# Kernel tuning notes

Hardware: AMD Instinct MI355X
Metric: run time of the kernel (lower is better)

The kernel has to match this reference:

```python
import jax, jax.numpy as jnp
import numpy as np


def setup_inputs() -> dict:
    key = jax.random.key(0)
    N, E, H, V, C, D, L = 10000, 50000, 128, 8, 5, 59, 2
    keys = iter(jax.random.split(key, 64))

    def p(*shape):
        return jax.random.normal(next(keys), shape, jnp.float32) * 0.05

    inp = dict(
        edge_index=jax.random.randint(next(keys), (2, E), 0, N),
        edge_attr=jax.random.normal(next(keys), (E, D), jnp.float32),
        delta_t=jnp.array([60.0], jnp.float32),
        memory=jnp.ones((N, H), jnp.float32),
        # edge_embed
        W_ee=p(H, D), b_ee=p(H),
        # edge_weight_gen
        W_ewg=p(V, 2 * H), b_ewg=p(V),
        # multi-view GIN convs (L layers, shared MLP across views)
        gin_W1=p(L, H, H), gin_b1=p(L, H), gin_W2=p(L, H, H), gin_b2=p(L, H),
        # Bochner time encoder
        W_t=p(H, 1), b_t=p(H),
        # GRUCell (torch gate order r,z,n)
        W_ih=p(3 * H, H), b_ih=p(3 * H), W_hh=p(3 * H, H), b_hh=p(3 * H),
        # update_nn (feeds detached memory only; not in returned outputs)
        W_up=p(H, V * H), b_up=p(H),
        # local attention (kdim=vdim=2H, 1 head)
        Wq_l=p(H, H), bq_l=p(H), Wk_l=p(H, 2 * H), bk_l=p(H),
        Wv_l=p(H, 2 * H), bv_l=p(H), Wo_l=p(H, H), bo_l=p(H),
        # global attention (1 head)
        Wq_g=p(H, H), bq_g=p(H), Wk_g=p(H, H), bk_g=p(H),
        Wv_g=p(H, H), bv_g=p(H), Wo_g=p(H, H), bo_g=p(H),
        # classifier MLP
        Wc1=p(H, 3 * H), bc1=p(H), Wc2=p(C, H), bc2=p(C),
    )
    return inp


def reference(edge_index, edge_attr, delta_t, memory,
              W_ee, b_ee, W_ewg, b_ewg,
              gin_W1, gin_b1, gin_W2, gin_b2,
              W_t, b_t, W_ih, b_ih, W_hh, b_hh, W_up, b_up,
              Wq_l, bq_l, Wk_l, bk_l, Wv_l, bv_l, Wo_l, bo_l,
              Wq_g, bq_g, Wk_g, bk_g, Wv_g, bv_g, Wo_g, bo_g,
              Wc1, bc1, Wc2, bc2):
    relu = jax.nn.relu
    N, H = memory.shape
    V = W_ewg.shape[0]
    L = gin_W1.shape[0]

    # ---- snapshot encoder (MultiGraphLayer) ----
    ea = relu(edge_attr @ W_ee.T + b_ee)                               # [E,H]
    src0, dst0 = edge_index[0], edge_index[1]
    ew = jax.nn.sigmoid(
        jnp.concatenate([ea, memory[src0]], -1) @ W_ewg.T + b_ewg)     # [E,V]
    h = jnp.broadcast_to(memory[:, None, :], (N, V, H))                # [N,V,H]
    cs, cd = dst0, src0  # edge_index flipped before convs (edge_index[[1,0]])
    for l in range(L):
        # multi-view GIN: view-weighted message + residual MLP update
        msg = relu(h[cs] + ea[:, None, :]) * ew[:, :, None]            # [E,V,H]
        agg = jax.ops.segment_sum(msg, cd, num_segments=N)             # [N,V,H]
        upd = relu((h + agg) @ gin_W1[l].T + gin_b1[l]) @ gin_W2[l].T + gin_b2[l]
        h = h + upd
    h_before = h

    # ---- GRU memory update (vectorized over the V 'class' slots) ----
    te = jnp.sin(delta_t[:, None] * W_t[:, 0] + b_t)                   # [1,H]
    x_in = h + te                                                      # [N,V,H]
    gi = x_in @ W_ih.T + b_ih                                          # [N,V,3H]
    gh = (memory @ W_hh.T + b_hh)[:, None, :]                          # [N,1,3H]
    r = jax.nn.sigmoid(gi[..., :H] + gh[..., :H])
    z = jax.nn.sigmoid(gi[..., H:2 * H] + gh[..., H:2 * H])
    n = jnp.tanh(gi[..., 2 * H:] + r * gh[..., 2 * H:])
    h_new = (1.0 - z) * n + z * memory[:, None, :]                     # [N,V,H]

    # ---- global/local attention fusion ----
    scale = 1.0 / jnp.sqrt(jnp.asarray(H, jnp.float32))
    sf, df = h_new[src0], h_new[dst0]                                  # [E,V,H]
    Wk1, Wk2 = Wk_l[:, :H], Wk_l[:, H:]  # split cat([src,dst]) projection
    Wv1, Wv2 = Wv_l[:, :H], Wv_l[:, H:]
    q_l = ea @ Wq_l.T + bq_l                                           # [E,H]
    K_l = sf @ Wk1.T + df @ Wk2.T + bk_l                               # [E,V,H]
    V_l = sf @ Wv1.T + df @ Wv2.T + bv_l
    a_l = jax.nn.softmax(jnp.einsum('eh,evh->ev', q_l, K_l) * scale, -1)
    local_out = jnp.einsum('ev,evh->eh', a_l, V_l) @ Wo_l.T + bo_l     # [E,H]

    pooled = h_new.mean(axis=0)                                        # [V,H]
    q_g = ea @ Wq_g.T + bq_g
    K_g = pooled @ Wk_g.T + bk_g
    V_g = pooled @ Wv_g.T + bv_g
    a_g = jax.nn.softmax((q_g @ K_g.T) * scale, axis=-1)               # [E,V]
    global_out = (a_g @ V_g) @ Wo_g.T + bo_g                           # [E,H]

    combined = jnp.concatenate([ea, local_out, global_out], axis=-1)   # [E,3H]
    logits = relu(combined @ Wc1.T + bc1) @ Wc2.T + bc2                # [E,C]
    return (logits, ew, h_before, a_g[:, None, :])
```

## Files before the change

### kernel.cpp

```cpp
#include <hip/hip_runtime.h>
#include <cstddef>


#define HSZ 128
typedef unsigned short ushortT;
typedef unsigned int uintT;
typedef short short8 __attribute__((ext_vector_type(8)));
typedef float f32x4 __attribute__((ext_vector_type(4)));

__device__ __forceinline__ float sigm(float x) { return 1.f / (1.f + __expf(-x)); }

__device__ __forceinline__ ushortT f2bf(float f) {
  unsigned int u = __float_as_uint(f);
  u += 0x7fffu + ((u >> 16) & 1u);
  return (ushortT)(u >> 16);
}
__device__ __forceinline__ float bf2f(ushortT u) {
  return __uint_as_float(((unsigned int)u) << 16);
}
__device__ __forceinline__ float bflo(uintT u) { return __uint_as_float(u << 16); }
__device__ __forceinline__ float bfhi(uintT u) { return __uint_as_float(u & 0xffff0000u); }
__device__ __forceinline__ uintT pk2bf(float a, float b) {
  return ((uintT)f2bf(b) << 16) | (uintT)f2bf(a);
}

__device__ __forceinline__ int swzA(int row, int chunk) {
  return row * 64 + (((chunk ^ row) & 7) << 3);
}
__device__ __forceinline__ int swzT(int row, int chunk) {
  return row * 128 + (((chunk & 8) | ((chunk ^ row) & 7)) << 3);
}

template<int ASRC, int ACT, bool OUTBF, bool ABF, bool WBF>
__global__ __launch_bounds__(256) void gemm_bf(
    const void* __restrict__ A1, const void* __restrict__ A2, const void* __restrict__ A3,
    const void* __restrict__ W, const float* __restrict__ bias,
    void* __restrict__ out_, int M, int K, int Nout)
{
  __shared__ short Ash[128 * 64];
  __shared__ short Bsh[128 * 64];
  float* out = (float*)out_;
  ushortT* outh = (ushortT*)out_;
  const int tid = threadIdx.x;
  const int m0 = blockIdx.x * 128;
  const int n0 = blockIdx.y * 128;
  const int l = tid & 63, w = tid >> 6;
  const int wr = w >> 1, wc = w & 1;
  const int lr = l & 15, lq = l >> 4;
  f32x4 acc[4][4] = {};

  for (int k0 = 0; k0 < K; k0 += 64) {
    __syncthreads();
    const bool fast = (k0 + 64 <= K);
    #pragma unroll
    for (int i = 0; i < 4; ++i) {
      int c = i * 256 + tid;
      int row = c >> 3, seg = c & 7;
      int kb = k0 + seg * 8;
      {
        int m = m0 + row;
        short8 pk;
        if (ABF) {
          if (m < M) {
            if (ASRC == 3) {
              const ushortT* S = (kb < 128) ? (const ushortT*)A1
                               : (kb < 256) ? (const ushortT*)A2 : (const ushortT*)A3;
              pk = *reinterpret_cast<const short8*>(S + (size_t)m * 128 + (kb & 127));
            } else {
              pk = *reinterpret_cast<const short8*>((const ushortT*)A1 + (size_t)m * K + kb);
            }
          } else {
            #pragma unroll
            for (int j = 0; j < 8; ++j) pk[j] = 0;
          }
        } else {
          const float* A1f = (const float*)A1;
          float v[8];
          if (fast && m < M) {
            const float4* p = reinterpret_cast<const float4*>(A1f + (size_t)m * K + kb);
            float4 x0 = p[0], x1 = p[1];
            v[0]=x0.x; v[1]=x0.y; v[2]=x0.z; v[3]=x0.w;
            v[4]=x1.x; v[5]=x1.y; v[6]=x1.z; v[7]=x1.w;
          } else {
            #pragma unroll
            for (int j = 0; j < 8; ++j) {
              int k = kb + j;
              v[j] = (m < M && k < K) ? A1f[(size_t)m * K + k] : 0.f;
            }
          }
          #pragma unroll
          for (int j = 0; j < 8; ++j) pk[j] = (short)f2bf(v[j]);
        }
        *reinterpret_cast<short8*>(&Ash[swzA(row, seg)]) = pk;
      }
      {
        int nn = n0 + row;
        short8 pk;
        if (WBF) {
          if (nn < Nout)
            pk = *reinterpret_cast<const short8*>((const ushortT*)W + (size_t)nn * K + kb);
          else {
            #pragma unroll
            for (int j = 0; j < 8; ++j) pk[j] = 0;
          }
        } else {
          const float* Wf = (const float*)W;
          float v[8];
          if (fast && nn < Nout) {
            const float4* p = reinterpret_cast<const float4*>(Wf + (size_t)nn * K + kb);
            float4 x0 = p[0], x1 = p[1];
            v[0]=x0.x; v[1]=x0.y; v[2]=x0.z; v[3]=x0.w;
            v[4]=x1.x; v[5]=x1.y; v[6]=x1.z; v[7]=x1.w;
          } else {
            #pragma unroll
            for (int j = 0; j < 8; ++j) {
              int k = kb + j;
              v[j] = (nn < Nout && k < K) ? Wf[(size_t)nn * K + k] : 0.f;
            }
          }
          #pragma unroll
          for (int j = 0; j < 8; ++j) pk[j] = (short)f2bf(v[j]);
        }
        *reinterpret_cast<short8*>(&Bsh[swzA(row, seg)]) = pk;
      }
    }
    __syncthreads();
    #pragma unroll
    for (int ks = 0; ks < 2; ++ks) {
      short8 a[4], b[4];
      #pragma unroll
      for (int mi = 0; mi < 4; ++mi)
        a[mi] = *reinterpret_cast<const short8*>(&Ash[swzA(wr*64 + mi*16 + lr, ks*4 + lq)]);
      #pragma unroll
      for (int ni = 0; ni < 4; ++ni)
        b[ni] = *reinterpret_cast<const short8*>(&Bsh[swzA(wc*64 + ni*16 + lr, ks*4 + lq)]);
      #pragma unroll
      for (int mi = 0; mi < 4; ++mi)
        #pragma unroll
        for (int ni = 0; ni < 4; ++ni)
          acc[mi][ni] = __builtin_amdgcn_mfma_f32_16x16x32_bf16(a[mi], b[ni], acc[mi][ni], 0, 0, 0);
    }
  }
  #pragma unroll
  for (int ni = 0; ni < 4; ++ni) {
    int col = n0 + wc*64 + ni*16 + lr;
    if (col >= Nout) continue;
    float bz = bias ? bias[col] : 0.f;
    #pragma unroll
    for (int mi = 0; mi < 4; ++mi) {
      int mb = m0 + wr*64 + mi*16 + lq*4;
      #pragma unroll
      for (int r = 0; r < 4; ++r) {
        int m = mb + r;
        if (m >= M) continue;
        float vv = acc[mi][ni][r] + bz;
        if (ACT == 1) vv = fmaxf(vv, 0.f);
        size_t o = (size_t)m * Nout + col;
        if (OUTBF) outh[o] = f2bf(vv); else out[o] = vv;
      }
    }
  }
}

template<int LMODE>
__global__ __launch_bounds__(256) void k_gin(
    const ushortT* __restrict__ hb, const ushortT* __restrict__ aggb,
    float* __restrict__ houtf, ushortT* __restrict__ houtb,
    const ushortT* __restrict__ W1b, const float* __restrict__ b1,
    const ushortT* __restrict__ W2b, const float* __restrict__ b2, int M)
{
  __shared__ short smem[24576];
  short* Ash  = smem;
  short* Bsh  = smem + 8192;
  short* Tsh  = smem;
  short* B2sh = smem + 16384;
  const int tid = threadIdx.x;
  const int m0 = blockIdx.x * 128;
  const int l = tid & 63, w = tid >> 6;
  const int wr = w >> 1, wc = w & 1;
  const int lr = l & 15, lq = l >> 4;
  f32x4 acc[4][4] = {};

  for (int ks2 = 0; ks2 < 2; ++ks2) {
    if (ks2) __syncthreads();
    #pragma unroll
    for (int i = 0; i < 4; ++i) {
      int c = i * 256 + tid;
      int row = c >> 3, seg = c & 7;
      int kb = ks2 * 64 + seg * 8;
      {
        int m = m0 + row;
        short8 pk;
        if (m < M) {
          short8 hv;
          if (LMODE == 1) hv = *reinterpret_cast<const short8*>(hb + ((size_t)(m >> 3)) * 128 + kb);
          else            hv = *reinterpret_cast<const short8*>(hb + (size_t)m * 128 + kb);
          short8 av = *reinterpret_cast<const short8*>(aggb + (size_t)m * 128 + kb);
          #pragma unroll
          for (int j = 0; j < 8; ++j)
            pk[j] = (short)f2bf(bf2f((ushortT)hv[j]) + bf2f((ushortT)av[j]));
        } else {
          #pragma unroll
          for (int j = 0; j < 8; ++j) pk[j] = 0;
        }
        *reinterpret_cast<short8*>(&Ash[swzA(row, seg)]) = pk;
      }
      *reinterpret_cast<short8*>(&Bsh[swzA(row, seg)]) =
          *reinterpret_cast<const short8*>(W1b + (size_t)row * 128 + kb);
      if (ks2 == 0)
        *reinterpret_cast<short8*>(&B2sh[swzA(row, seg)]) =
            *reinterpret_cast<const short8*>(W2b + (size_t)row * 128 + seg * 8);
    }
    __syncthreads();
    #pragma unroll
    for (int ks = 0; ks < 2; ++ks) {
      short8 a[4], b[4];
      #pragma unroll
      for (int mi = 0; mi < 4; ++mi)
        a[mi] = *reinterpret_cast<const short8*>(&Ash[swzA(wr*64 + mi*16 + lr, ks*4 + lq)]);
      #pragma unroll
      for (int ni = 0; ni < 4; ++ni)
        b[ni] = *reinterpret_cast<const short8*>(&Bsh[swzA(wc*64 + ni*16 + lr, ks*4 + lq)]);
      #pragma unroll
      for (int mi = 0; mi < 4; ++mi)
        #pragma unroll
        for (int ni = 0; ni < 4; ++ni)
          acc[mi][ni] = __builtin_amdgcn_mfma_f32_16x16x32_bf16(a[mi], b[ni], acc[mi][ni], 0, 0, 0);
    }
  }
  __syncthreads();
  {
    float b1v[4];
    #pragma unroll
    for (int ni = 0; ni < 4; ++ni) b1v[ni] = b1[wc*64 + ni*16 + lr];
    #pragma unroll
    for (int mi = 0; mi < 4; ++mi)
      #pragma unroll
      for (int ni = 0; ni < 4; ++ni) {
        int col = wc*64 + ni*16 + lr;
        #pragma unroll
        for (int r = 0; r < 4; ++r) {
          int row = wr*64 + mi*16 + lq*4 + r;
          float v = fmaxf(acc[mi][ni][r] + b1v[ni], 0.f);
          Tsh[swzT(row, col >> 3) + (col & 7)] = (short)f2bf(v);
        }
      }
  }
  __syncthreads();
  f32x4 acc2[4][4] = {};
  for (int ks2 = 0; ks2 < 2; ++ks2) {
    if (ks2) {
      __syncthreads();
      #pragma unroll
      for (int i = 0; i < 4; ++i) {
        int c = i * 256 + tid;
        int row = c >> 3, seg = c & 7;
        *reinterpret_cast<short8*>(&B2sh[swzA(row, seg)]) =
            *reinterpret_cast<const short8*>(W2b + (size_t)row * 128 + 64 + seg * 8);
      }
      __syncthreads();
    }
    #pragma unroll
    for (int ks = 0; ks < 2; ++ks) {
      short8 a[4], b[4];
      #pragma unroll
      for (int mi = 0; mi < 4; ++mi)
        a[mi] = *reinterpret_cast<const short8*>(&Tsh[swzT(wr*64 + mi*16 + lr, ks2*8 + ks*4 + lq)]);
      #pragma unroll
      for (int ni = 0; ni < 4; ++ni)
        b[ni] = *reinterpret_cast<const short8*>(&B2sh[swzA(wc*64 + ni*16 + lr, ks*4 + lq)]);
      #pragma unroll
      for (int mi = 0; mi < 4; ++mi)
        #pragma unroll
        for (int ni = 0; ni < 4; ++ni)
          acc2[mi][ni] = __builtin_amdgcn_mfma_f32_16x16x32_bf16(a[mi], b[ni], acc2[mi][ni], 0, 0, 0);
    }
  }
  {
    float b2v[4];
    #pragma unroll
    for (int ni = 0; ni < 4; ++ni) b2v[ni] = b2[wc*64 + ni*16 + lr];
    #pragma unroll
    for (int ni = 0; ni < 4; ++ni) {
      int col = wc*64 + ni*16 + lr;
      #pragma unroll
      for (int mi = 0; mi < 4; ++mi) {
        int mb = m0 + wr*64 + mi*16 + lq*4;
        #pragma unroll
        for (int r = 0; r < 4; ++r) {
          int m = mb + r;
          if (m >= M) continue;
          float base = (LMODE == 1) ? bf2f(hb[((size_t)(m >> 3)) * 128 + col])
                                    : bf2f(hb[(size_t)m * 128 + col]);
          float ho = base + acc2[mi][ni][r] + b2v[ni];
          if (LMODE == 1) houtb[(size_t)m * 128 + col] = f2bf(ho);
          else            houtf[(size_t)m * 128 + col] = ho;
        }
      }
    }
  }
}

__global__ __launch_bounds__(512) void k_giru(
    const float* __restrict__ hf, const float* __restrict__ te,
    const ushortT* __restrict__ Wihb, const float* __restrict__ b_ih,
    const ushortT* __restrict__ ghb, const ushortT* __restrict__ memb,
    ushortT* __restrict__ hnb, int M)
{
  __shared__ short Ash[8192];
  __shared__ short Bsh[24576];
  const int tid = threadIdx.x;
  const int m0 = blockIdx.x * 64;
  const int l = tid & 63, w = tid >> 6;
  const int lr = l & 15, lq = l >> 4;
  const int r0 = (w >> 1) * 16, c0 = (w & 1) * 64;
  f32x4 acc[3][4] = {};

  #pragma unroll
  for (int i = 0; i < 2; ++i) {
    int c = i * 512 + tid;
    int row = c >> 4, seg = c & 15;
    int m = m0 + row;
    short8 pk;
    if (m < M) {
      const float4* p = reinterpret_cast<const float4*>(hf + (size_t)m * 128 + seg * 8);
      const float4* t = reinterpret_cast<const float4*>(te + seg * 8);
      float4 x0 = p[0], x1 = p[1], t0 = t[0], t1 = t[1];
      pk[0]=(short)f2bf(x0.x+t0.x); pk[1]=(short)f2bf(x0.y+t0.y);
      pk[2]=(short)f2bf(x0.z+t0.z); pk[3]=(short)f2bf(x0.w+t0.w);
      pk[4]=(short)f2bf(x1.x+t1.x); pk[5]=(short)f2bf(x1.y+t1.y);
      pk[6]=(short)f2bf(x1.z+t1.z); pk[7]=(short)f2bf(x1.w+t1.w);
    } else {
      #pragma unroll
      for (int j = 0; j < 8; ++j) pk[j] = 0;
    }
    *reinterpret_cast<short8*>(&Ash[swzT(row, seg)]) = pk;
  }
  for (int ks2 = 0; ks2 < 2; ++ks2) {
    if (ks2) __syncthreads();
    #pragma unroll
    for (int i = 0; i < 6; ++i) {
      int c = i * 512 + tid;
      int row = c >> 3, seg = c & 7;
      *reinterpret_cast<short8*>(&Bsh[swzA(row, seg)]) =
          *reinterpret_cast<const short8*>(Wihb + (size_t)row * 128 + ks2 * 64 + seg * 8);
    }
    __syncthreads();
    #pragma unroll
    for (int ks = 0; ks < 2; ++ks) {
      short8 a = *reinterpret_cast<const short8*>(&Ash[swzT(r0 + lr, ks2*8 + ks*4 + lq)]);
      #pragma unroll
      for (int s = 0; s < 3; ++s)
        #pragma unroll
        for (int xi = 0; xi < 4; ++xi) {
          short8 b = *reinterpret_cast<const short8*>(
              &Bsh[swzA(s*128 + c0 + xi*16 + lr, ks*4 + lq)]);
          acc[s][xi] = __builtin_amdgcn_mfma_f32_16x16x32_bf16(a, b, acc[s][xi], 0, 0, 0);
        }
    }
  }
  #pragma unroll
  for (int xi = 0; xi < 4; ++xi) {
    int x = c0 + xi * 16 + lr;
    float br = b_ih[x], bz = b_ih[128 + x], bn = b_ih[256 + x];
    #pragma unroll
    for (int rr = 0; rr < 4; ++rr) {
      int m = m0 + r0 + lq * 4 + rr;
      if (m >= M) continue;
      int node = m >> 3;
      float ghr = bf2f(ghb[(size_t)node * 384 + x]);
      float ghz = bf2f(ghb[(size_t)node * 384 + 128 + x]);
      float ghn = bf2f(ghb[(size_t)node * 384 + 256 + x]);
      float mem = bf2f(memb[(size_t)node * 128 + x]);
      float rv = sigm(acc[0][xi][rr] + br + ghr);
      float zv = sigm(acc[1][xi][rr] + bz + ghz);
      float nv = tanhf(acc[2][xi][rr] + bn + rv * ghn);
      hnb[(size_t)m * 128 + x] = f2bf((1.f - zv) * nv + zv * mem);
    }
  }
}

__global__ void k_hist(const int* __restrict__ srcI, int* __restrict__ cnt, int E)
{
  int e = blockIdx.x * 256 + threadIdx.x;
  if (e < E) atomicAdd(&cnt[srcI[e]], 1);
}

__global__ __launch_bounds__(1024) void k_scan(const int* __restrict__ cnt,
    int* __restrict__ ofs, int* __restrict__ cur, int N)
{
  __shared__ int buf[1024];
  __shared__ int carry;
  int tid = threadIdx.x;
  if (tid == 0) carry = 0;
  __syncthreads();
  for (int base = 0; base < N; base += 1024) {
    int i = base + tid;
    int v = (i < N) ? cnt[i] : 0;
    buf[tid] = v;
    __syncthreads();
    for (int off = 1; off < 1024; off <<= 1) {
      int t = (tid >= off) ? buf[tid - off] : 0;
      __syncthreads();
      buf[tid] += t;
      __syncthreads();
    }
    int excl = carry + buf[tid] - v;
    if (i < N) { ofs[i] = excl; cur[i] = excl; }
    __syncthreads();
    if (tid == 0) carry += buf[1023];
    __syncthreads();
  }
  if (tid == 0) ofs[N] = carry;
}

__global__ void k_fill(const int* __restrict__ srcI, int* __restrict__ cur,
                       int* __restrict__ eid, int E)
{
  int e = blockIdx.x * 256 + threadIdx.x;
  if (e >= E) return;
  int p = atomicAdd(&cur[srcI[e]], 1);
  eid[p] = e;
}

template<int LMODE>
__global__ __launch_bounds__(256) void k_agg(const ushortT* __restrict__ hb,
    const ushortT* __restrict__ eab, const float* __restrict__ ew,
    const int* __restrict__ dstI, const int* __restrict__ ofs,
    const int* __restrict__ eid, ushortT* __restrict__ aggb, int N)
{
  int half = threadIdx.x >> 7;
  int x = threadIdx.x & 127;
  int n = blockIdx.x * 2 + half;
  if (n >= N) return;
  float acc[8] = {};
  int beg = ofs[n], end = ofs[n + 1];
  for (int i = beg; i < end; ++i) {
    int e = eid[i];
    int d = dstI[e];
    float eav = bf2f(eab[(size_t)e * 128 + x]);
    const float* ewp = ew + (size_t)e * 8;
    if (LMODE == 1) {
      float m = fmaxf(bf2f(hb[(size_t)d * 128 + x]) + eav, 0.f);
      #pragma unroll
      for (int v = 0; v < 8; ++v) acc[v] += m * ewp[v];
    } else {
      const ushortT* hd = hb + (size_t)d * 1024;
      #pragma unroll
      for (int v = 0; v < 8; ++v)
        acc[v] += fmaxf(bf2f(hd[v * 128 + x]) + eav, 0.f) * ewp[v];
    }
  }
  ushortT* ag = aggb + (size_t)n * 1024;
  #pragma unroll
  for (int v = 0; v < 8; ++v) ag[v * 128 + x] = f2bf(acc[v]);
}

__global__ __launch_bounds__(256) void k_ew(const ushortT* __restrict__ eab,
    const ushortT* __restrict__ memb, const int* __restrict__ srcI,
    const float* __restrict__ W_ewg, const float* __restrict__ b_ewg,
    float* __restrict__ ew, int E)
{
  __shared__ float Wsh[2048];
  __shared__ float bsh[8];
  int tid = threadIdx.x;
  for (int i = tid; i < 2048; i += 256) Wsh[i] = W_ewg[i];
  if (tid < 8) bsh[tid] = b_ewg[tid];
  __syncthreads();
  int wv = tid >> 6, lane = tid & 63;
  int e = blockIdx.x * 4 + wv;
  if (e >= E) return;
  int s = srcI[e];
  float c0 = bf2f(eab[(size_t)e * 128 + lane]);
  float c1 = bf2f(eab[(size_t)e * 128 + 64 + lane]);
  float c2 = bf2f(memb[(size_t)s * 128 + lane]);
  float c3 = bf2f(memb[(size_t)s * 128 + 64 + lane]);
  #pragma unroll
  for (int v = 0; v < 8; ++v) {
    float p = c0 * Wsh[v * 256 + lane] + c1 * Wsh[v * 256 + 64 + lane]
            + c2 * Wsh[v * 256 + 128 + lane] + c3 * Wsh[v * 256 + 192 + lane];
    #pragma unroll
    for (int o = 32; o; o >>= 1) p += __shfl_down(p, o);
    if (lane == 0) ew[(size_t)e * 8 + v] = sigm(p + bsh[v]);
  }
}

__global__ void k_cvt(const float* __restrict__ src, ushortT* __restrict__ dst, int total)
{
  int i = blockIdx.x * 256 + threadIdx.x;
  if (i < total) dst[i] = f2bf(src[i]);
}

__global__ void k_te(const float* __restrict__ delta_t, const float* __restrict__ W_t,
                     const float* __restrict__ b_t, float* __restrict__ te)
{
  int t = threadIdx.x;
  if (t < 128) te[t] = sinf(delta_t[0] * W_t[t] + b_t[t]);
}

__global__ __launch_bounds__(256) void k_pool(const ushortT* __restrict__ hnb,
                                              float* __restrict__ prw, int N)
{
  int tid = threadIdx.x;
  float acc[4] = {0.f, 0.f, 0.f, 0.f};
  for (int n = blockIdx.x; n < N; n += gridDim.x) {
    const ushortT* row = hnb + (size_t)n * 1024;
    #pragma unroll
    for (int j = 0; j < 4; ++j) acc[j] += bf2f(row[tid + j * 256]);
  }
  #pragma unroll
  for (int j = 0; j < 4; ++j) atomicAdd(&prw[tid + j * 256], acc[j]);
}

__global__ __launch_bounds__(256) void k_prep(
    const float* __restrict__ Wo_l, const float* __restrict__ Wv_l,
    const float* __restrict__ bv_l, const float* __restrict__ bo_l,
    const float* __restrict__ Wq_l, const float* __restrict__ bq_l,
    const float* __restrict__ Wk_l, const float* __restrict__ Wq_g,
    const float* __restrict__ bq_g,
    ushortT* __restrict__ Wl2b, float* __restrict__ blv,
    ushortT* __restrict__ Wqkgb, float* __restrict__ bqkg)
{
  int idx = blockIdx.x * 256 + threadIdx.x;
  if (idx < 32768) {
    int n = idx >> 8, k = idx & 255;
    float a = 0.f;
    for (int j = 0; j < 128; ++j) a += Wo_l[n * 128 + j] * Wv_l[j * 256 + k];
    Wl2b[idx] = f2bf(a);
  } else if (idx < 65536) {
    int rem = idx - 32768;
    int n = rem >> 7, j = rem & 127;
    float a = 0.f;
    for (int k = 0; k < 128; ++k) a += Wq_l[k * 128 + j] * Wk_l[k * 256 + n];
    Wqkgb[rem] = f2bf(a);
  } else {
    int rem = idx - 65536;
    Wqkgb[32768 + rem] = f2bf(Wq_g[rem]);
  }
  if (blockIdx.x == 0 && threadIdx.x < 128) {
    int n = threadIdx.x;
    float a = bo_l[n];
    for (int j = 0; j < 128; ++j) a += Wo_l[n * 128 + j] * bv_l[j];
    blv[n] = a;
  }
  if (blockIdx.x == 1) {
    int n = threadIdx.x;
    float a = 0.f;
    for (int k = 0; k < 128; ++k) a += bq_l[k] * Wk_l[k * 256 + n];
    bqkg[n] = a;
  }
  if (blockIdx.x == 2 && threadIdx.x < 128) bqkg[256 + threadIdx.x] = bq_g[threadIdx.x];
}

__global__ __launch_bounds__(256) void k_kgg(const float* __restrict__ prw,
    const float* __restrict__ Wk_g, const float* __restrict__ Wv_g, const float* __restrict__ bv_g,
    const float* __restrict__ Wo_g, float* __restrict__ Kg, float* __restrict__ G, int N)
{
  __shared__ float pl[1024];
  __shared__ float vg[1024];
  int tid = threadIdx.x;
  float invN = 1.f / (float)N;
  for (int i = tid; i < 1024; i += 256) pl[i] = prw[i] * invN;
  __syncthreads();
  for (int o = tid; o < 1024; o += 256) {
    int v = o >> 7, x = o & 127;
    float a = 0.f, b = 0.f;
    for (int k = 0; k < 128; ++k) {
      float p = pl[v * 128 + k];
      a += p * Wk_g[(size_t)x * 128 + k];
      b += p * Wv_g[(size_t)x * 128 + k];
    }
    Kg[o] = a;
    vg[o] = b + bv_g[x];
  }
  __syncthreads();
  for (int o = tid; o < 1024; o += 256) {
    int v = o >> 7, x = o & 127;
    float a = 0.f;
    for (int k = 0; k < 128; ++k) a += vg[v * 128 + k] * Wo_g[(size_t)x * 128 + k];
    G[o] = a;
  }
}

__global__ __launch_bounds__(256) void k_lg(
    const ushortT* __restrict__ hnb, const ushortT* __restrict__ qkgb,
    const int* __restrict__ srcI, const int* __restrict__ dstI,
    const float* __restrict__ Kg, const float* __restrict__ G,
    const float* __restrict__ bo_g,
    float* __restrict__ ag_out, ushortT* __restrict__ wsd,
    ushortT* __restrict__ glbb, int E)
{
  __shared__ float Kgs[1024], Gs[1024], bs[128];
  int tid = threadIdx.x;
  for (int i = tid; i < 1024; i += 256) { Kgs[i] = Kg[i]; Gs[i] = G[i]; }
  if (tid < 128) bs[tid] = bo_g[tid];
  __syncthreads();
  int w = tid >> 6, l = tid & 63;
  int e = blockIdx.x * 4 + w;
  if (e >= E) return;
  int s = srcI[e], d = dstI[e];
  const uintT* qrow = reinterpret_cast<const uintT*>(qkgb + (size_t)e * 384);
  const uintT* srow = reinterpret_cast<const uintT*>(hnb + (size_t)s * 1024);
  const uintT* drow = reinterpret_cast<const uintT*>(hnb + (size_t)d * 1024);
  uintT q1u = qrow[l], q2u = qrow[64 + l], qgu = qrow[128 + l];
  float q1a = bflo(q1u), q1b = bfhi(q1u);
  float q2a = bflo(q2u), q2b = bfhi(q2u);
  float qga = bflo(qgu), qgb_ = bfhi(qgu);
  float sfa[8], sfb[8], dfa[8], dfb[8], pl[8], pg[8];
  #pragma unroll
  for (int v = 0; v < 8; ++v) {
    uintT su = srow[v * 64 + l], du = drow[v * 64 + l];
    sfa[v] = bflo(su); sfb[v] = bfhi(su);
    dfa[v] = bflo(du); dfb[v] = bfhi(du);
    pl[v] = q1a * sfa[v] + q1b * sfb[v] + q2a * dfa[v] + q2b * dfb[v];
    float2 kv = *reinterpret_cast<const float2*>(&Kgs[v * 128 + 2 * l]);
    pg[v] = qga * kv.x + qgb_ * kv.y;
  }
  #pragma unroll
  for (int v = 0; v < 8; ++v) {
    #pragma unroll
    for (int m = 1; m <= 32; m <<= 1) {
      pl[v] += __shfl_xor(pl[v], m);
      pg[v] += __shfl_xor(pg[v], m);
    }
  }
  const float scale = 0.08838834764831845f;
  float mx = pl[0];
  #pragma unroll
  for (int v = 1; v < 8; ++v) mx = fmaxf(mx, pl[v]);
  float suml = 0.f, al[8];
  #pragma unroll
  for (int v = 0; v < 8; ++v) { al[v] = __expf((pl[v] - mx) * scale); suml += al[v]; }
  float invl = 1.f / suml;
  float wsa = 0.f, wsb = 0.f, wda = 0.f, wdb = 0.f;
  #pragma unroll
  for (int v = 0; v < 8; ++v) {
    float a = al[v];
    wsa += a * sfa[v]; wsb += a * sfb[v];
    wda += a * dfa[v]; wdb += a * dfb[v];
  }
  uintT* wrow = reinterpret_cast<uintT*>(wsd + (size_t)e * 256);
  wrow[l]      = pk2bf(wsa * invl, wsb * invl);
  wrow[64 + l] = pk2bf(wda * invl, wdb * invl);
  float mg = pg[0];
  #pragma unroll
  for (int v = 1; v < 8; ++v) mg = fmaxf(mg, pg[v]);
  float sumg = 0.f, ag[8];
  #pragma unroll
  for (int v = 0; v < 8; ++v) { ag[v] = __expf((pg[v] - mg) * scale); sumg += ag[v]; }
  float invg = 1.f / sumg;
  if (l < 8) ag_out[(size_t)e * 8 + l] = ag[l] * invg;
  float2 bv = *reinterpret_cast<const float2*>(&bs[2 * l]);
  float ga = bv.x, gb = bv.y;
  #pragma unroll
  for (int v = 0; v < 8; ++v) {
    float sv = ag[v] * invg;
    float2 gv = *reinterpret_cast<const float2*>(&Gs[v * 128 + 2 * l]);
    ga += sv * gv.x; gb += sv * gv.y;
  }
  reinterpret_cast<uintT*>(glbb)[(size_t)e * 64 + l] = pk2bf(ga, gb);
}

__global__ __launch_bounds__(256) void k_logits(const ushortT* __restrict__ hid,
    const float* __restrict__ Wc2, const float* __restrict__ bc2,
    float* __restrict__ logits, int E)
{
  __shared__ float Wsh[640];
  __shared__ float bsh[5];
  int tid = threadIdx.x;
  for (int i = tid; i < 640; i += 256) Wsh[i] = Wc2[i];
  if (tid < 5) bsh[tid] = bc2[tid];
  __syncthreads();
  int wv = tid >> 6, lane = tid & 63;
  int e = blockIdx.x * 4 + wv;
  if (e >= E) return;
  float h0 = bf2f(hid[(size_t)e * 128 + lane]), h1 = bf2f(hid[(size_t)e * 128 + 64 + lane]);
  #pragma unroll
  for (int c = 0; c < 5; ++c) {
    float p = h0 * Wsh[c * 128 + lane] + h1 * Wsh[c * 128 + 64 + lane];
    #pragma unroll
    for (int o = 32; o; o >>= 1) p += __shfl_down(p, o);
    if (lane == 0) logits[(size_t)e * 5 + c] = p + bsh[c];
  }
}

extern "C" void kernel_launch(void* const* d_in, const int* in_sizes, int n_in,
                              void* d_out, int out_size, void* d_ws, size_t ws_size,
                              hipStream_t stream)
{
  const int*   edge_index = (const int*)d_in[0];
  const float* edge_attr  = (const float*)d_in[1];
  const float* delta_t    = (const float*)d_in[2];
  const float* memory     = (const float*)d_in[3];
  const float* W_ee  = (const float*)d_in[4];
  const float* b_ee  = (const float*)d_in[5];
  const float* W_ewg = (const float*)d_in[6];
  const float* b_ewg = (const float*)d_in[7];
  const float* gin_W1 = (const float*)d_in[8];
  const float* gin_b1 = (const float*)d_in[9];
  const float* gin_W2 = (const float*)d_in[10];
  const float* gin_b2 = (const float*)d_in[11];
  const float* W_t  = (const float*)d_in[12];
  const float* b_t  = (const float*)d_in[13];
  const float* W_ih = (const float*)d_in[14];
  const float* b_ih = (const float*)d_in[15];
  const float* W_hh = (const float*)d_in[16];
  const float* b_hh = (const float*)d_in[17];
  const float* Wq_l = (const float*)d_in[20];
  const float* bq_l = (const float*)d_in[21];
  const float* Wk_l = (const float*)d_in[22];
  const float* Wv_l = (const float*)d_in[24];
  const float* bv_l = (const float*)d_in[25];
  const float* Wo_l = (const float*)d_in[26];
  const float* bo_l = (const float*)d_in[27];
  const float* Wq_g = (const float*)d_in[28];
  const float* bq_g = (const float*)d_in[29];
  const float* Wk_g = (const float*)d_in[30];
  const float* Wv_g = (const float*)d_in[32];
  const float* bv_g = (const float*)d_in[33];
  const float* Wo_g = (const float*)d_in[34];
  const float* bo_g = (const float*)d_in[35];
  const float* Wc1  = (const float*)d_in[36];
  const float* bc1  = (const float*)d_in[37];
  const float* Wc2  = (const float*)d_in[38];
  const float* bc2  = (const float*)d_in[39];

  const int E = in_sizes[0] / 2;
  const int N = in_sizes[3] / HSZ;
  const int* srcI = edge_index;
  const int* dstI = edge_index + E;

  float* out    = (float*)d_out;
  float* logits = out;
  float* ew     = out + (size_t)E * 5;
  float* h      = out + (size_t)E * 13;
  float* ag_out = out + (size_t)E * 13 + (size_t)N * 1024;

  float* ws = (float*)d_ws;
  size_t off = 0;
  auto alloc = [&](size_t n) { size_t o = off; off += (n + 255) & ~(size_t)255; return o; };
  float* te   = ws + alloc(128);
  float* blv  = ws + alloc(128);
  float* bqkg = ws + alloc(384);
  float* Kg   = ws + alloc(1024);
  float* G    = ws + alloc(1024);
  float* prw  = ws + alloc(1024);
  int* cnt = (int*)(ws + alloc(N));
  int* ofs = (int*)(ws + alloc(N + 1));
  int* cur = (int*)(ws + alloc(N));
  int* eid = (int*)(ws + alloc(E));
  ushortT* memb   = (ushortT*)(ws + alloc((size_t)N * 64));
  ushortT* eab    = (ushortT*)(ws + alloc((size_t)E * 64));
  ushortT* h1b    = (ushortT*)(ws + alloc((size_t)N * 512));
  ushortT* hnb    = (ushortT*)(ws + alloc((size_t)N * 512));
  ushortT* ghb    = (ushortT*)(ws + alloc((size_t)N * 192));
  ushortT* ginW1b = (ushortT*)(ws + alloc(16384));
  ushortT* ginW2b = (ushortT*)(ws + alloc(16384));
  ushortT* Wihb   = (ushortT*)(ws + alloc(24576));
  ushortT* Wc1b   = (ushortT*)(ws + alloc(24576));
  ushortT* Wl2b   = (ushortT*)(ws + alloc(16384));
  ushortT* Wqkgb  = (ushortT*)(ws + alloc(24576));
  size_t brA = (size_t)N * 512, brC = (size_t)E * 448;
  size_t brsz = brA > brC ? brA : brC;
  float* BR = ws + alloc(brsz);
  if (ws_size < off * sizeof(float)) return;

  ushortT* aggb = (ushortT*)BR;
  ushortT* qkgb = (ushortT*)BR;
  ushortT* wsd  = (ushortT*)(BR + (size_t)E * 192);
  ushortT* lclb = (ushortT*)(BR + (size_t)E * 320);
  ushortT* glbb = (ushortT*)(BR + (size_t)E * 384);
  ushortT* hid  = (ushortT*)BR;

  auto cdiv = [](int a, int b) { return (a + b - 1) / b; };

  hipMemsetAsync(cnt, 0, (size_t)N * sizeof(int), stream);
  k_hist<<<cdiv(E, 256), 256, 0, stream>>>(srcI, cnt, E);
  k_scan<<<1, 1024, 0, stream>>>(cnt, ofs, cur, N);
  k_fill<<<cdiv(E, 256), 256, 0, stream>>>(srcI, cur, eid, E);
  k_cvt<<<cdiv(N * 128, 256), 256, 0, stream>>>(memory, memb, N * 128);
  k_cvt<<<128, 256, 0, stream>>>(gin_W1, ginW1b, 32768);
  k_cvt<<<128, 256, 0, stream>>>(gin_W2, ginW2b, 32768);
  k_cvt<<<192, 256, 0, stream>>>(W_ih, Wihb, 49152);
  k_cvt<<<192, 256, 0, stream>>>(Wc1, Wc1b, 49152);
  gemm_bf<0, 1, true, false, false><<<dim3(cdiv(E, 128), 1), 256, 0, stream>>>(
      edge_attr, nullptr, nullptr, W_ee, b_ee, eab, E, 59, 128);
  k_ew<<<cdiv(E, 4), 256, 0, stream>>>(eab, memb, srcI, W_ewg, b_ewg, ew, E);
  k_te<<<1, 128, 0, stream>>>(delta_t, W_t, b_t, te);
  k_prep<<<320, 256, 0, stream>>>(Wo_l, Wv_l, bv_l, bo_l, Wq_l, bq_l, Wk_l, Wq_g, bq_g,
                                  Wl2b, blv, Wqkgb, bqkg);
  gemm_bf<0, 0, true, false, false><<<dim3(cdiv(N, 128), 3), 256, 0, stream>>>(
      memory, nullptr, nullptr, W_hh, b_hh, ghb, N, 128, 384);
  k_agg<1><<<cdiv(N, 2), 256, 0, stream>>>(memb, eab, ew, dstI, ofs, eid, aggb, N);
  k_gin<1><<<cdiv(N * 8, 128), 256, 0, stream>>>(
      memb, aggb, nullptr, h1b, ginW1b, gin_b1, ginW2b, gin_b2, N * 8);
  k_agg<2><<<cdiv(N, 2), 256, 0, stream>>>(h1b, eab, ew, dstI, ofs, eid, aggb, N);
  k_gin<2><<<cdiv(N * 8, 128), 256, 0, stream>>>(
      h1b, aggb, h, nullptr, ginW1b + 16384, gin_b1 + 128,
      ginW2b + 16384, gin_b2 + 128, N * 8);
  k_giru<<<cdiv(N * 8, 64), 512, 0, stream>>>(h, te, Wihb, b_ih, ghb, memb, hnb, N * 8);
  hipMemsetAsync(prw, 0, 1024 * sizeof(float), stream);
  k_pool<<<256, 256, 0, stream>>>(hnb, prw, N);
  k_kgg<<<1, 256, 0, stream>>>(prw, Wk_g, Wv_g, bv_g, Wo_g, Kg, G, N);
  gemm_bf<0, 0, true, true, true><<<dim3(cdiv(E, 128), 3), 256, 0, stream>>>(
      eab, nullptr, nullptr, Wqkgb, bqkg, qkgb, E, 128, 384);
  k_lg<<<cdiv(E, 4), 256, 0, stream>>>(hnb, qkgb, srcI, dstI, Kg, G, bo_g,
                                       ag_out, wsd, glbb, E);
  gemm_bf<0, 0, true, true, true><<<dim3(cdiv(E, 128), 1), 256, 0, stream>>>(
      wsd, nullptr, nullptr, Wl2b, blv, lclb, E, 256, 128);
  gemm_bf<3, 1, true, true, true><<<dim3(cdiv(E, 128), 1), 256, 0, stream>>>(
      eab, lclb, glbb, Wc1b, bc1, hid, E, 384, 128);
  k_logits<<<cdiv(E, 4), 256, 0, stream>>>(hid, Wc2, bc2, logits, E);
}
```

Baseline: 542.8 us.

## Fold local value/output and global query-key projections into weights; fuse pooling and conversions

Precomputes Wc1·Wo·Wv so the local-attention output GEMM is removed, and the classifier GEMM reads the weighted src/dst features directly with K=512. Folds the global query-key product into a small 8-column extension of the Q projection via a new k_sc kernel, which shrinks that GEMM output from 384 to 264 columns. Mean pooling moves into the GRU kernel through shared-memory and global atomics, and the time encoder and weight conversions are merged into fewer kernels. k_lg now handles two edges per wave. The changes remove launches and intermediate traffic, but add extra precompute kernels and change the rounding points of bf16 values.

```diff
diff --git a/kernel.cpp b/kernel.cpp
--- a/kernel.cpp
+++ b/kernel.cpp
@@ -62,10 +62,13 @@
         short8 pk;
         if (ABF) {
           if (m < M) {
-            if (ASRC == 3) {
-              const ushortT* S = (kb < 128) ? (const ushortT*)A1
-                               : (kb < 256) ? (const ushortT*)A2 : (const ushortT*)A3;
-              pk = *reinterpret_cast<const short8*>(S + (size_t)m * 128 + (kb & 127));
+            if (ASRC == 4) {
+              if (kb < 128)
+                pk = *reinterpret_cast<const short8*>((const ushortT*)A1 + (size_t)m * 128 + kb);
+              else if (kb < 384)
+                pk = *reinterpret_cast<const short8*>((const ushortT*)A2 + (size_t)m * 256 + (kb - 128));
+              else
+                pk = *reinterpret_cast<const short8*>((const ushortT*)A3 + (size_t)m * 128 + (kb - 384));
             } else {
               pk = *reinterpret_cast<const short8*>((const ushortT*)A1 + (size_t)m * K + kb);
             }
@@ -305,10 +308,11 @@
     const float* __restrict__ hf, const float* __restrict__ te,
     const ushortT* __restrict__ Wihb, const float* __restrict__ b_ih,
     const ushortT* __restrict__ ghb, const ushortT* __restrict__ memb,
-    ushortT* __restrict__ hnb, int M)
+    ushortT* __restrict__ hnb, float* __restrict__ prw, int M)
 {
   __shared__ short Ash[8192];
   __shared__ short Bsh[24576];
+  float* poolsh = reinterpret_cast<float*>(Ash);
   const int tid = threadIdx.x;
   const int m0 = blockIdx.x * 64;
   const int l = tid & 63, w = tid >> 6;
@@ -359,6 +363,9 @@
         }
     }
   }
+  __syncthreads();
+  for (int i = tid; i < 1024; i += 512) poolsh[i] = 0.f;
+  __syncthreads();
   #pragma unroll
   for (int xi = 0; xi < 4; ++xi) {
     int x = c0 + xi * 16 + lr;
@@ -375,9 +382,13 @@
       float rv = sigm(acc[0][xi][rr] + br + ghr);
       float zv = sigm(acc[1][xi][rr] + bz + ghz);
       float nv = tanhf(acc[2][xi][rr] + bn + rv * ghn);
-      hnb[(size_t)m * 128 + x] = f2bf((1.f - zv) * nv + zv * mem);
-    }
-  }
+      float hn = (1.f - zv) * nv + zv * mem;
+      hnb[(size_t)m * 128 + x] = f2bf(hn);
+      atomicAdd(&poolsh[(m & 7) * 128 + x], hn);
+    }
+  }
+  __syncthreads();
+  for (int i = tid; i < 1024; i += 512) atomicAdd(&prw[i], poolsh[i]);
 }
 
 __global__ void k_hist(const int* __restrict__ srcI, int* __restrict__ cnt, int E)
@@ -485,57 +496,43 @@
   }
 }
 
-__global__ void k_cvt(const float* __restrict__ src, ushortT* __restrict__ dst, int total)
+__global__ void k_cvtall(const float* __restrict__ s0, ushortT* __restrict__ d0, int n0,
+                         const float* __restrict__ s1, ushortT* __restrict__ d1, int n1,
+                         const float* __restrict__ s2, ushortT* __restrict__ d2, int n2,
+                         const float* __restrict__ s3, ushortT* __restrict__ d3, int n3)
 {
   int i = blockIdx.x * 256 + threadIdx.x;
-  if (i < total) dst[i] = f2bf(src[i]);
-}
-
-__global__ void k_te(const float* __restrict__ delta_t, const float* __restrict__ W_t,
-                     const float* __restrict__ b_t, float* __restrict__ te)
-{
-  int t = threadIdx.x;
-  if (t < 128) te[t] = sinf(delta_t[0] * W_t[t] + b_t[t]);
-}
-
-__global__ __launch_bounds__(256) void k_pool(const ushortT* __restrict__ hnb,
-                                              float* __restrict__ prw, int N)
-{
-  int tid = threadIdx.x;
-  float acc[4] = {0.f, 0.f, 0.f, 0.f};
-  for (int n = blockIdx.x; n < N; n += gridDim.x) {
-    const ushortT* row = hnb + (size_t)n * 1024;
-    #pragma unroll
-    for (int j = 0; j < 4; ++j) acc[j] += bf2f(row[tid + j * 256]);
-  }
-  #pragma unroll
-  for (int j = 0; j < 4; ++j) atomicAdd(&prw[tid + j * 256], acc[j]);
+  if (i < n0) { d0[i] = f2bf(s0[i]); return; }
+  i -= n0;
+  if (i < n1) { d1[i] = f2bf(s1[i]); return; }
+  i -= n1;
+  if (i < n2) { d2[i] = f2bf(s2[i]); return; }
+  i -= n2;
+  if (i < n3) d3[i] = f2bf(s3[i]);
 }
 
 __global__ __launch_bounds__(256) void k_prep(
     const float* __restrict__ Wo_l, const float* __restrict__ Wv_l,
     const float* __restrict__ bv_l, const float* __restrict__ bo_l,
     const float* __restrict__ Wq_l, const float* __restrict__ bq_l,
-    const float* __restrict__ Wk_l, const float* __restrict__ Wq_g,
-    const float* __restrict__ bq_g,
-    ushortT* __restrict__ Wl2b, float* __restrict__ blv,
-    ushortT* __restrict__ Wqkgb, float* __restrict__ bqkg)
+    const float* __restrict__ Wk_l,
+    const float* __restrict__ delta_t, const float* __restrict__ W_t,
+    const float* __restrict__ b_t,
+    float* __restrict__ Wl2f, float* __restrict__ blv,
+    ushortT* __restrict__ Wqkgb, float* __restrict__ bqkg, float* __restrict__ te)
 {
   int idx = blockIdx.x * 256 + threadIdx.x;
   if (idx < 32768) {
     int n = idx >> 8, k = idx & 255;
     float a = 0.f;
     for (int j = 0; j < 128; ++j) a += Wo_l[n * 128 + j] * Wv_l[j * 256 + k];
-    Wl2b[idx] = f2bf(a);
-  } else if (idx < 65536) {
+    Wl2f[idx] = a;
+  } else {
     int rem = idx - 32768;
     int n = rem >> 7, j = rem & 127;
     float a = 0.f;
     for (int k = 0; k < 128; ++k) a += Wq_l[k * 128 + j] * Wk_l[k * 256 + n];
     Wqkgb[rem] = f2bf(a);
-  } else {
-    int rem = idx - 65536;
-    Wqkgb[32768 + rem] = f2bf(Wq_g[rem]);
   }
   if (blockIdx.x == 0 && threadIdx.x < 128) {
     int n = threadIdx.x;
@@ -549,7 +546,33 @@
     for (int k = 0; k < 128; ++k) a += bq_l[k] * Wk_l[k * 256 + n];
     bqkg[n] = a;
   }
-  if (blockIdx.x == 2 && threadIdx.x < 128) bqkg[256 + threadIdx.x] = bq_g[threadIdx.x];
+  if (blockIdx.x == 2 && threadIdx.x < 128) {
+    int t = threadIdx.x;
+    te[t] = sinf(delta_t[0] * W_t[t] + b_t[t]);
+  }
+}
+
+__global__ __launch_bounds__(256) void k_prep2(
+    const float* __restrict__ Wc1, const float* __restrict__ bc1,
+    const float* __restrict__ Wl2f, const float* __restrict__ blv,
+    ushortT* __restrict__ Wc1p, float* __restrict__ bc1p)
+{
+  int idx = blockIdx.x * 256 + threadIdx.x;
+  int n = idx >> 9, k = idx & 511;
+  float a;
+  if (k < 128) a = Wc1[(size_t)n * 384 + k];
+  else if (k < 384) {
+    int kk = k - 128;
+    a = 0.f;
+    for (int j = 0; j < 128; ++j) a += Wc1[(size_t)n * 384 + 128 + j] * Wl2f[j * 256 + kk];
+  } else a = Wc1[(size_t)n * 384 + 256 + (k - 384)];
+  Wc1p[idx] = f2bf(a);
+  if (blockIdx.x == 0 && threadIdx.x < 128) {
+    int nn = threadIdx.x;
+    float b = bc1[nn];
+    for (int j = 0; j < 128; ++j) b += Wc1[(size_t)nn * 384 + 128 + j] * blv[j];
+    bc1p[nn] = b;
+  }
 }
 
 __global__ __launch_bounds__(256) void k_kgg(const float* __restrict__ prw,
@@ -582,83 +605,107 @@
   }
 }
 
+__global__ __launch_bounds__(256) void k_sc(const float* __restrict__ Kg,
+    const float* __restrict__ Wq_g, const float* __restrict__ bq_g,
+    ushortT* __restrict__ Wqkgb, float* __restrict__ bqkg)
+{
+  int idx = blockIdx.x * 256 + threadIdx.x;
+  int v = idx >> 7, j = idx & 127;
+  float a = 0.f;
+  for (int x = 0; x < 128; ++x) a += Kg[v * 128 + x] * Wq_g[(size_t)x * 128 + j];
+  Wqkgb[(size_t)(256 + v) * 128 + j] = f2bf(a);
+  if (blockIdx.x == 0 && threadIdx.x < 8) {
+    int vv = threadIdx.x;
+    float b = 0.f;
+    for (int x = 0; x < 128; ++x) b += bq_g[x] * Kg[vv * 128 + x];
+    bqkg[256 + vv] = b;
+  }
+}
+
 __global__ __launch_bounds__(256) void k_lg(
     const ushortT* __restrict__ hnb, const ushortT* __restrict__ qkgb,
     const int* __restrict__ srcI, const int* __restrict__ dstI,
-    const float* __restrict__ Kg, const float* __restrict__ G,
-    const float* __restrict__ bo_g,
+    const float* __restrict__ G, const float* __restrict__ bo_g,
     float* __restrict__ ag_out, ushortT* __restrict__ wsd,
     ushortT* __restrict__ glbb, int E)
 {
-  __shared__ float Kgs[1024], Gs[1024], bs[128];
+  __shared__ float Gs[1024], bsh[128];
   int tid = threadIdx.x;
-  for (int i = tid; i < 1024; i += 256) { Kgs[i] = Kg[i]; Gs[i] = G[i]; }
-  if (tid < 128) bs[tid] = bo_g[tid];
-  __syncthreads();
-  int w = tid >> 6, l = tid & 63;
-  int e = blockIdx.x * 4 + w;
-  if (e >= E) return;
-  int s = srcI[e], d = dstI[e];
-  const uintT* qrow = reinterpret_cast<const uintT*>(qkgb + (size_t)e * 384);
-  const uintT* srow = reinterpret_cast<const uintT*>(hnb + (size_t)s * 1024);
-  const uintT* drow = reinterpret_cast<const uintT*>(hnb + (size_t)d * 1024);
-  uintT q1u = qrow[l], q2u = qrow[64 + l], qgu = qrow[128 + l];
-  float q1a = bflo(q1u), q1b = bfhi(q1u);
-  float q2a = bflo(q2u), q2b = bfhi(q2u);
-  float qga = bflo(qgu), qgb_ = bfhi(qgu);
-  float sfa[8], sfb[8], dfa[8], dfb[8], pl[8], pg[8];
+  for (int i = tid; i < 1024; i += 256) Gs[i] = G[i];
+  if (tid < 128) bsh[tid] = bo_g[tid];
+  __syncthreads();
+  int w = tid >> 6, l = tid & 63, half = l >> 5, l31 = l & 31;
+  int e = blockIdx.x * 8 + w * 2 + half;
+  int ec = (e < E) ? e : (E - 1);
+  int s = srcI[ec], d = dstI[ec];
+  const uint2* qrow = reinterpret_cast<const uint2*>(qkgb + (size_t)ec * 264);
+  uint2 q1u = qrow[l31], q2u = qrow[32 + l31];
+  uint4 scu = *reinterpret_cast<const uint4*>(qkgb + (size_t)ec * 264 + 256);
+  const uint2* srow = reinterpret_cast<const uint2*>(hnb + (size_t)s * 1024);
+  const uint2* drow = reinterpret_cast<const uint2*>(hnb + (size_t)d * 1024);
+  uint2 su[8], du[8];
+  #pragma unroll
+  for (int v = 0; v < 8; ++v) { su[v] = srow[v * 32 + l31]; du[v] = drow[v * 32 + l31]; }
+  float q1f[4] = {bflo(q1u.x), bfhi(q1u.x), bflo(q1u.y), bfhi(q1u.y)};
+  float q2f[4] = {bflo(q2u.x), bfhi(q2u.x), bflo(q2u.y), bfhi(q2u.y)};
+  float pl[8];
   #pragma unroll
   for (int v = 0; v < 8; ++v) {
-    uintT su = srow[v * 64 + l], du = drow[v * 64 + l];
-    sfa[v] = bflo(su); sfb[v] = bfhi(su);
-    dfa[v] = bflo(du); dfb[v] = bfhi(du);
-    pl[v] = q1a * sfa[v] + q1b * sfb[v] + q2a * dfa[v] + q2b * dfb[v];
-    float2 kv = *reinterpret_cast<const float2*>(&Kgs[v * 128 + 2 * l]);
-    pg[v] = qga * kv.x + qgb_ * kv.y;
+    pl[v] = q1f[0] * bflo(su[v].x) + q1f[1] * bfhi(su[v].x)
+          + q1f[2] * bflo(su[v].y) + q1f[3] * bfhi(su[v].y)
+          + q2f[0] * bflo(du[v].x) + q2f[1] * bfhi(du[v].x)
+          + q2f[2] * bflo(du[v].y) + q2f[3] * bfhi(du[v].y);
   }
   #pragma unroll
   for (int v = 0; v < 8; ++v) {
     #pragma unroll
-    for (int m = 1; m <= 32; m <<= 1) {
-      pl[v] += __shfl_xor(pl[v], m);
-      pg[v] += __shfl_xor(pg[v], m);
-    }
+    for (int m = 1; m <= 16; m <<= 1) pl[v] += __shfl_xor(pl[v], m);
   }
   const float scale = 0.08838834764831845f;
-  float mx = pl[0];
-  #pragma unroll
-  for (int v = 1; v < 8; ++v) mx = fmaxf(mx, pl[v]);
+  float mx = fmaxf(fmaxf(fmaxf(pl[0], pl[1]), fmaxf(pl[2], pl[3])),
+                   fmaxf(fmaxf(pl[4], pl[5]), fmaxf(pl[6], pl[7])));
   float suml = 0.f, al[8];
   #pragma unroll
   for (int v = 0; v < 8; ++v) { al[v] = __expf((pl[v] - mx) * scale); suml += al[v]; }
   float invl = 1.f / suml;
-  float wsa = 0.f, wsb = 0.f, wda = 0.f, wdb = 0.f;
+  float ws0 = 0.f, ws1 = 0.f, ws2 = 0.f, ws3 = 0.f;
+  float wd0 = 0.f, wd1 = 0.f, wd2 = 0.f, wd3 = 0.f;
   #pragma unroll
   for (int v = 0; v < 8; ++v) {
     float a = al[v];
-    wsa += a * sfa[v]; wsb += a * sfb[v];
-    wda += a * dfa[v]; wdb += a * dfb[v];
-  }
-  uintT* wrow = reinterpret_cast<uintT*>(wsd + (size_t)e * 256);
-  wrow[l]      = pk2bf(wsa * invl, wsb * invl);
-  wrow[64 + l] = pk2bf(wda * invl, wdb * invl);
-  float mg = pg[0];
-  #pragma unroll
-  for (int v = 1; v < 8; ++v) mg = fmaxf(mg, pg[v]);
+    ws0 += a * bflo(su[v].x); ws1 += a * bfhi(su[v].x);
+    ws2 += a * bflo(su[v].y); ws3 += a * bfhi(su[v].y);
+    wd0 += a * bflo(du[v].x); wd1 += a * bfhi(du[v].x);
+    wd2 += a * bflo(du[v].y); wd3 += a * bfhi(du[v].y);
+  }
+  if (e < E) {
+    uint2* wrow = reinterpret_cast<uint2*>(wsd + (size_t)e * 256);
+    uint2 t0; t0.x = pk2bf(ws0 * invl, ws1 * invl); t0.y = pk2bf(ws2 * invl, ws3 * invl);
+    uint2 t1; t1.x = pk2bf(wd0 * invl, wd1 * invl); t1.y = pk2bf(wd2 * invl, wd3 * invl);
+    wrow[l31] = t0;
+    wrow[32 + l31] = t1;
+  }
+  float sg[8] = {bflo(scu.x), bfhi(scu.x), bflo(scu.y), bfhi(scu.y),
+                 bflo(scu.z), bfhi(scu.z), bflo(scu.w), bfhi(scu.w)};
+  float mg = fmaxf(fmaxf(fmaxf(sg[0], sg[1]), fmaxf(sg[2], sg[3])),
+                   fmaxf(fmaxf(sg[4], sg[5]), fmaxf(sg[6], sg[7])));
   float sumg = 0.f, ag[8];
   #pragma unroll
-  for (int v = 0; v < 8; ++v) { ag[v] = __expf((pg[v] - mg) * scale); sumg += ag[v]; }
+  for (int v = 0; v < 8; ++v) { ag[v] = __expf((sg[v] - mg) * scale); sumg += ag[v]; }
   float invg = 1.f / sumg;
-  if (l < 8) ag_out[(size_t)e * 8 + l] = ag[l] * invg;
-  float2 bv = *reinterpret_cast<const float2*>(&bs[2 * l]);
-  float ga = bv.x, gb = bv.y;
+  if (e < E && l31 < 8) ag_out[(size_t)e * 8 + l31] = ag[l31] * invg;
+  float4 b4 = *reinterpret_cast<const float4*>(&bsh[4 * l31]);
+  float g0 = b4.x, g1 = b4.y, g2 = b4.z, g3 = b4.w;
   #pragma unroll
   for (int v = 0; v < 8; ++v) {
     float sv = ag[v] * invg;
-    float2 gv = *reinterpret_cast<const float2*>(&Gs[v * 128 + 2 * l]);
-    ga += sv * gv.x; gb += sv * gv.y;
-  }
-  reinterpret_cast<uintT*>(glbb)[(size_t)e * 64 + l] = pk2bf(ga, gb);
+    float4 gv = *reinterpret_cast<const float4*>(&Gs[v * 128 + 4 * l31]);
+    g0 += sv * gv.x; g1 += sv * gv.y; g2 += sv * gv.z; g3 += sv * gv.w;
+  }
+  if (e < E) {
+    uint2 t; t.x = pk2bf(g0, g1); t.y = pk2bf(g2, g3);
+    reinterpret_cast<uint2*>(glbb + (size_t)e * 128)[l31] = t;
+  }
 }
 
 __global__ __launch_bounds__(256) void k_logits(const ushortT* __restrict__ hid,
@@ -742,6 +789,7 @@
   float* te   = ws + alloc(128);
   float* blv  = ws + alloc(128);
   float* bqkg = ws + alloc(384);
+  float* bc1p = ws + alloc(128);
   float* Kg   = ws + alloc(1024);
   float* G    = ws + alloc(1024);
   float* prw  = ws + alloc(1024);
@@ -757,38 +805,39 @@
   ushortT* ginW1b = (ushortT*)(ws + alloc(16384));
   ushortT* ginW2b = (ushortT*)(ws + alloc(16384));
   ushortT* Wihb   = (ushortT*)(ws + alloc(24576));
-  ushortT* Wc1b   = (ushortT*)(ws + alloc(24576));
-  ushortT* Wl2b   = (ushortT*)(ws + alloc(16384));
-  ushortT* Wqkgb  = (ushortT*)(ws + alloc(24576));
-  size_t brA = (size_t)N * 512, brC = (size_t)E * 448;
+  float*   Wl2f   = ws + alloc(32768);
+  ushortT* Wc1p   = (ushortT*)(ws + alloc(32768));
+  ushortT* Wqkgb  = (ushortT*)(ws + alloc(16896));
+  size_t brA = (size_t)N * 512, brC = (size_t)E * 324;
   size_t brsz = brA > brC ? brA : brC;
   float* BR = ws + alloc(brsz);
   if (ws_size < off * sizeof(float)) return;
 
   ushortT* aggb = (ushortT*)BR;
   ushortT* qkgb = (ushortT*)BR;
-  ushortT* wsd  = (ushortT*)(BR + (size_t)E * 192);
-  ushortT* lclb = (ushortT*)(BR + (size_t)E * 320);
-  ushortT* glbb = (ushortT*)(BR + (size_t)E * 384);
+  ushortT* wsd  = (ushortT*)(BR + (size_t)E * 132);
+  ushortT* glbb = (ushortT*)(BR + (size_t)E * 260);
   ushortT* hid  = (ushortT*)BR;
 
   auto cdiv = [](int a, int b) { return (a + b - 1) / b; };
 
   hipMemsetAsync(cnt, 0, (size_t)N * sizeof(int), stream);
+  hipMemsetAsync(prw, 0, 1024 * sizeof(float), stream);
   k_hist<<<cdiv(E, 256), 256, 0, stream>>>(srcI, cnt, E);
   k_scan<<<1, 1024, 0, stream>>>(cnt, ofs, cur, N);
   k_fill<<<cdiv(E, 256), 256, 0, stream>>>(srcI, cur, eid, E);
-  k_cvt<<<cdiv(N * 128, 256), 256, 0, stream>>>(memory, memb, N * 128);
-  k_cvt<<<128, 256, 0, stream>>>(gin_W1, ginW1b, 32768);
-  k_cvt<<<128, 256, 0, stream>>>(gin_W2, ginW2b, 32768);
-  k_cvt<<<192, 256, 0, stream>>>(W_ih, Wihb, 49152);
-  k_cvt<<<192, 256, 0, stream>>>(Wc1, Wc1b, 49152);
+  {
+    int total = N * 128 + 32768 + 32768 + 49152;
+    k_cvtall<<<cdiv(total, 256), 256, 0, stream>>>(
+        memory, memb, N * 128, gin_W1, ginW1b, 32768,
+        gin_W2, ginW2b, 32768, W_ih, Wihb, 49152);
+  }
   gemm_bf<0, 1, true, false, false><<<dim3(cdiv(E, 128), 1), 256, 0, stream>>>(
       edge_attr, nullptr, nullptr, W_ee, b_ee, eab, E, 59, 128);
   k_ew<<<cdiv(E, 4), 256, 0, stream>>>(eab, memb, srcI, W_ewg, b_ewg, ew, E);
-  k_te<<<1, 128, 0, stream>>>(delta_t, W_t, b_t, te);
-  k_prep<<<320, 256, 0, stream>>>(Wo_l, Wv_l, bv_l, bo_l, Wq_l, bq_l, Wk_l, Wq_g, bq_g,
-                                  Wl2b, blv, Wqkgb, bqkg);
+  k_prep<<<256, 256, 0, stream>>>(Wo_l, Wv_l, bv_l, bo_l, Wq_l, bq_l, Wk_l,
+                                  delta_t, W_t, b_t, Wl2f, blv, Wqkgb, bqkg, te);
+  k_prep2<<<256, 256, 0, stream>>>(Wc1, bc1, Wl2f, blv, Wc1p, bc1p);
   gemm_bf<0, 0, true, false, false><<<dim3(cdiv(N, 128), 3), 256, 0, stream>>>(
       memory, nullptr, nullptr, W_hh, b_hh, ghb, N, 128, 384);
   k_agg<1><<<cdiv(N, 2), 256, 0, stream>>>(memb, eab, ew, dstI, ofs, eid, aggb, N);
@@ -798,17 +847,14 @@
   k_gin<2><<<cdiv(N * 8, 128), 256, 0, stream>>>(
       h1b, aggb, h, nullptr, ginW1b + 16384, gin_b1 + 128,
       ginW2b + 16384, gin_b2 + 128, N * 8);
-  k_giru<<<cdiv(N * 8, 64), 512, 0, stream>>>(h, te, Wihb, b_ih, ghb, memb, hnb, N * 8);
-  hipMemsetAsync(prw, 0, 1024 * sizeof(float), stream);
-  k_pool<<<256, 256, 0, stream>>>(hnb, prw, N);
+  k_giru<<<cdiv(N * 8, 64), 512, 0, stream>>>(h, te, Wihb, b_ih, ghb, memb, hnb, prw, N * 8);
   k_kgg<<<1, 256, 0, stream>>>(prw, Wk_g, Wv_g, bv_g, Wo_g, Kg, G, N);
+  k_sc<<<4, 256, 0, stream>>>(Kg, Wq_g, bq_g, Wqkgb, bqkg);
   gemm_bf<0, 0, true, true, true><<<dim3(cdiv(E, 128), 3), 256, 0, stream>>>(
-      eab, nullptr, nullptr, Wqkgb, bqkg, qkgb, E, 128, 384);
-  k_lg<<<cdiv(E, 4), 256, 0, stream>>>(hnb, qkgb, srcI, dstI, Kg, G, bo_g,
+      eab, nullptr, nullptr, Wqkgb, bqkg, qkgb, E, 128, 264);
+  k_lg<<<cdiv(E, 8), 256, 0, stream>>>(hnb, qkgb, srcI, dstI, G, bo_g,
                                        ag_out, wsd, glbb, E);
-  gemm_bf<0, 0, true, true, true><<<dim3(cdiv(E, 128), 1), 256, 0, stream>>>(
-      wsd, nullptr, nullptr, Wl2b, blv, lclb, E, 256, 128);
-  gemm_bf<3, 1, true, true, true><<<dim3(cdiv(E, 128), 1), 256, 0, stream>>>(
-      eab, lclb, glbb, Wc1b, bc1, hid, E, 384, 128);
+  gemm_bf<4, 1, true, true, true><<<dim3(cdiv(E, 128), 1), 256, 0, stream>>>(
+      eab, wsd, glbb, Wc1p, bc1p, hid, E, 512, 128);
   k_logits<<<cdiv(E, 4), 256, 0, stream>>>(hid, Wc2, bc2, logits, E);
 }
```

New measurement: 535.5 us. Within noise of the previous version (-1.3%).
